# Performance work log

Hardware: AMD Instinct MI355X
Metric: run time of the kernel (lower is better)

## Reference

```python
import jax, jax.numpy as jnp
import numpy as np

N_NODES = 100000   # embedding table rows
FEAT = 512         # feat_dim F
BATCH = 8192       # seed nodes per batch
DEG = 32           # sampled neighbors per node (col 0 = self)
BN_EPS = 1e-5


def setup_inputs() -> dict:
    key = jax.random.key(0)
    ks = jax.random.split(key, 6)
    feat_table = jax.random.normal(ks[0], (N_NODES, FEAT), dtype=jnp.float32)
    W_gen = jax.random.normal(ks[1], (2 * FEAT, 2 * FEAT), dtype=jnp.float32) * 0.02
    weight1 = jax.random.normal(ks[2], (3 * FEAT, 3 * FEAT), dtype=jnp.float32) * 0.02
    gamma = jnp.ones((3 * FEAT,), dtype=jnp.float32)
    beta = jnp.zeros((3 * FEAT,), dtype=jnp.float32)
    nodes = jax.random.randint(ks[3], (BATCH,), 0, N_NODES, dtype=jnp.int32)
    neigh_idx = jax.random.randint(ks[4], (BATCH, DEG), 0, N_NODES, dtype=jnp.int32)
    neigh_idx = neigh_idx.at[:, 0].set(nodes)  # self node included, as in samp_neighs
    return {"feat_table": feat_table, "W_gen": W_gen, "weight1": weight1,
            "gamma": gamma, "beta": beta, "nodes": nodes, "neigh_idx": neigh_idx}


def _batchnorm_train(x, gamma, beta):
    # BatchNorm1d in training mode: biased batch statistics over axis 0
    mu = x.mean(axis=0)
    var = x.var(axis=0)
    return (x - mu) * jax.lax.rsqrt(var + BN_EPS) * gamma + beta


def _gen(x, W_gen):
    # generator module: raw = x @ W_gen, gen = relu(raw) (shape-preserving [B,2F])
    raw = x @ W_gen
    return jax.nn.relu(raw), raw


def reference(feat_table, W_gen, weight1, gamma, beta, nodes, neigh_idx):
    # self features: [B, F]
    self_feats = feat_table[nodes]
    # gather neighbor feats [B, K, F] and mean-pool (replaces dense mask.mm)
    neigh_feats = feat_table[neigh_idx]
    agg_feats = neigh_feats.mean(axis=1)                 # [B, F]
    cat_feats = jnp.concatenate([self_feats, agg_feats], axis=1)  # [B, 2F]
    gen_feats, raw_feats = _gen(cat_feats, W_gen)        # [B, 2F] each

    # environment aggregation: self node (column 0) removed from neighbor set
    env_agg_feats = neigh_feats[:, 1:, :].mean(axis=1)   # [B, F]
    env_cat = jnp.concatenate([jnp.zeros_like(self_feats), env_agg_feats], axis=1)
    env_gen_feats, env_raw_feats = _gen(env_cat, W_gen)

    # train_flag=True, rl_train_flag=False path
    feats = jnp.concatenate([agg_feats, gen_feats], axis=1)  # [B, 3F]
    to_feats = jax.nn.relu(_batchnorm_train(feats, gamma, beta) @ weight1)
    return (agg_feats, to_feats, gen_feats, raw_feats, env_gen_feats, env_raw_feats)
```

## Files before the change

### kernel.cpp

```cpp
#include <hip/hip_runtime.h>
#include <hip/hip_bf16.h>

typedef unsigned short u16;
typedef unsigned int u32;
typedef __attribute__((ext_vector_type(8))) short short8;
typedef __attribute__((ext_vector_type(4))) float f32x4;

#define BATCH 8192
#define FEAT 512
#define DEG 32
#define BM 128
#define BN 128
#define BK 32

__device__ __forceinline__ float b2f(u16 h){
  union { u32 u; float f; } x; x.u = ((u32)h) << 16; return x.f;
}
__device__ __forceinline__ u16 f2b(float f){
  __hip_bfloat16 h = __float2bfloat16(f);
  return *reinterpret_cast<u16*>(&h);
}
__device__ __forceinline__ u32 pack2(float lo, float hi){
  return (u32)f2b(lo) | (((u32)f2b(hi)) << 16);
}

__device__ __forceinline__ f32x4 mfma_bf16_16x16x32(short8 a, short8 b, f32x4 c){
  asm("v_mfma_f32_16x16x32_bf16 %0, %1, %2, %0" : "+v"(c) : "v"(a), "v"(b));
  return c;
}

__device__ __forceinline__ void gload16(const u16* g, u16* l){
  __builtin_amdgcn_global_load_lds(
      (const __attribute__((address_space(1))) u32*)(const void*)g,
      (__attribute__((address_space(3))) u32*)(void*)l, 16, 0, 0);
}

__global__ __launch_bounds__(256) void gather_agg(
    const float* __restrict__ feat, const int* __restrict__ nodes,
    const int* __restrict__ nidx, float* __restrict__ out_agg,
    u16* __restrict__ cat_bf, u16* __restrict__ env_bf)
{
  const int b = blockIdx.x;
  const int t = threadIdx.x;
  __shared__ int idx[DEG];
  __shared__ int self_node;
  if (t < DEG) idx[t] = nidx[b * DEG + t];
  if (t == 64) self_node = nodes[b];
  __syncthreads();
  const int f = t * 2;
  float s0 = 0.f, s1 = 0.f;
  #pragma unroll 8
  for (int k = 0; k < DEG; ++k){
    const float2 v = *(const float2*)(feat + (size_t)idx[k] * FEAT + f);
    s0 += v.x; s1 += v.y;
  }
  const float2 sv = *(const float2*)(feat + (size_t)self_node * FEAT + f);
  const float a0 = s0 * (1.f/32.f), a1 = s1 * (1.f/32.f);
  const float e0 = (s0 - sv.x) * (1.f/31.f), e1 = (s1 - sv.y) * (1.f/31.f);
  *(float2*)(out_agg + (size_t)b * FEAT + f) = make_float2(a0, a1);
  *(u32*)(cat_bf + (size_t)b * 1024 + f) = pack2(sv.x, sv.y);
  *(u32*)(cat_bf + (size_t)b * 1024 + FEAT + f) = pack2(a0, a1);
  *(u32*)(env_bf + (size_t)b * FEAT + f) = pack2(e0, e1);
}

__global__ __launch_bounds__(256) void transpose_f2b(
    const float* __restrict__ in, u16* __restrict__ out, int R, int C)
{
  __shared__ float tile[32][33];
  const int c0 = blockIdx.x * 32, r0 = blockIdx.y * 32;
  const int x = threadIdx.x, y = threadIdx.y;
  #pragma unroll
  for (int i = 0; i < 32; i += 8)
    tile[y + i][x] = in[(size_t)(r0 + y + i) * C + (c0 + x)];
  __syncthreads();
  #pragma unroll
  for (int i = 0; i < 32; i += 8)
    out[(size_t)(c0 + y + i) * R + (r0 + x)] = f2b(tile[x][y + i]);
}

template<bool WRITE_RAW>
__device__ __forceinline__ void gemm_body(
    const u16* __restrict__ A, int lda, const u16* __restrict__ BT, int ldb,
    int K, float* __restrict__ Craw, float* __restrict__ Crelu, int ldc,
    int m0, int n0, u16* As, u16* Bs)
{
  const int t = threadIdx.x;
  const int wave = t >> 6, lane = t & 63;
  const int wr = wave >> 1, wc = wave & 1;
  const int lm = lane & 15, quad = lane >> 4;

  const int sr = wave * 32 + (lane >> 2);
  const int sc = (lane & 3) * 8;

  f32x4 acc[4][4] = {};

  for (int k0 = 0; k0 < K; k0 += BK){
    gload16(A  + (size_t)(m0 + sr)      * lda + k0 + sc, As + sr * 32 + sc);
    gload16(A  + (size_t)(m0 + sr + 16) * lda + k0 + sc, As + (sr + 16) * 32 + sc);
    gload16(BT + (size_t)(n0 + sr)      * ldb + k0 + sc, Bs + sr * 32 + sc);
    gload16(BT + (size_t)(n0 + sr + 16) * ldb + k0 + sc, Bs + (sr + 16) * 32 + sc);
    __syncthreads();
    short8 af[4], bf[4];
    #pragma unroll
    for (int i = 0; i < 4; ++i)
      af[i] = *(const short8*)&As[(wr * 64 + i * 16 + lm) * 32 + quad * 8];
    #pragma unroll
    for (int j = 0; j < 4; ++j)
      bf[j] = *(const short8*)&Bs[(wc * 64 + j * 16 + lm) * 32 + quad * 8];
    #pragma unroll
    for (int i = 0; i < 4; ++i)
      #pragma unroll
      for (int j = 0; j < 4; ++j)
        acc[i][j] = mfma_bf16_16x16x32(af[i], bf[j], acc[i][j]);
    __syncthreads();
  }
  #pragma unroll
  for (int i = 0; i < 4; ++i){
    const int row = m0 + wr * 64 + i * 16 + quad * 4;
    #pragma unroll
    for (int j = 0; j < 4; ++j){
      const int col = n0 + wc * 64 + j * 16 + lm;
      #pragma unroll
      for (int r = 0; r < 4; ++r){
        const float v = acc[i][j][r];
        const size_t off = (size_t)(row + r) * ldc + col;
        if (WRITE_RAW) Craw[off] = v;
        Crelu[off] = fmaxf(v, 0.f);
      }
    }
  }
}

__global__ __launch_bounds__(256) void gemm12(
    const u16* __restrict__ catA, const u16* __restrict__ envA,
    const u16* __restrict__ wgT,
    float* __restrict__ raw, float* __restrict__ gen,
    float* __restrict__ envraw, float* __restrict__ envgen)
{
  __shared__ __align__(16) u16 As[BM * BK];
  __shared__ __align__(16) u16 Bs[BN * BK];
  const int z = blockIdx.z;
  const u16* A  = z ? envA : catA;
  const int lda = z ? 512 : 1024;
  const int K   = z ? 512 : 1024;
  const u16* BT = z ? wgT + 512 : wgT;
  float* Craw   = z ? envraw : raw;
  float* Crelu  = z ? envgen : gen;
  gemm_body<true>(A, lda, BT, 1024, K, Craw, Crelu, 1024,
                  blockIdx.y * BM, blockIdx.x * BN, As, Bs);
}

__global__ __launch_bounds__(256) void gemm3(
    const u16* __restrict__ bnA, const u16* __restrict__ w1T,
    float* __restrict__ to_out)
{
  __shared__ __align__(16) u16 As[BM * BK];
  __shared__ __align__(16) u16 Bs[BN * BK];
  gemm_body<false>(bnA, 1536, w1T, 1536, 1536, nullptr, to_out, 1536,
                   blockIdx.y * BM, blockIdx.x * BN, As, Bs);
}

__global__ __launch_bounds__(256) void zero_f32(float* __restrict__ p, int n){
  const int i = blockIdx.x * 256 + threadIdx.x;
  if (i < n) p[i] = 0.f;
}

__global__ __launch_bounds__(256) void bn_partial(
    const float* __restrict__ agg, const float* __restrict__ gen,
    float* __restrict__ sums)
{
  const int l = threadIdx.x & 63;
  const int ty = threadIdx.x >> 6;
  const int c = blockIdx.x * 64 + l;
  const int r0 = blockIdx.y * 1024;
  float s = 0.f, q = 0.f;
  if (c < 512){
    for (int r = r0 + ty; r < r0 + 1024; r += 4){
      const float x = agg[(size_t)r * 512 + c];
      s += x; q += x * x;
    }
  } else {
    for (int r = r0 + ty; r < r0 + 1024; r += 4){
      const float x = gen[(size_t)r * 1024 + (c - 512)];
      s += x; q += x * x;
    }
  }
  __shared__ float sh[2][4][64];
  sh[0][ty][l] = s; sh[1][ty][l] = q;
  __syncthreads();
  if (ty == 0){
    s = sh[0][0][l] + sh[0][1][l] + sh[0][2][l] + sh[0][3][l];
    q = sh[1][0][l] + sh[1][1][l] + sh[1][2][l] + sh[1][3][l];
    atomicAdd(&sums[c], s);
    atomicAdd(&sums[1536 + c], q);
  }
}

__global__ __launch_bounds__(256) void bn_finalize(
    const float* __restrict__ sums, const float* __restrict__ gamma,
    const float* __restrict__ beta, float* __restrict__ sArr, float* __restrict__ tArr)
{
  const int c = blockIdx.x * 256 + threadIdx.x;
  if (c >= 1536) return;
  const float mean = sums[c] * (1.f / 8192.f);
  const float var = sums[1536 + c] * (1.f / 8192.f) - mean * mean;
  const float rs = rsqrtf(var + 1e-5f);
  const float sc = gamma[c] * rs;
  sArr[c] = sc;
  tArr[c] = beta[c] - mean * sc;
}

__global__ __launch_bounds__(384) void prep_bnA(
    const float* __restrict__ agg, const float* __restrict__ gen,
    const float* __restrict__ sArr, const float* __restrict__ tArr,
    u16* __restrict__ bnA)
{
  const int m = blockIdx.x;
  const int t = threadIdx.x;
  const int c = t * 4;
  const float4 x = (c < 512)
      ? *(const float4*)(agg + (size_t)m * 512 + c)
      : *(const float4*)(gen + (size_t)m * 1024 + (c - 512));
  const float4 s4 = *(const float4*)(sArr + c);
  const float4 t4 = *(const float4*)(tArr + c);
  const u32 lo = pack2(fmaf(x.x, s4.x, t4.x), fmaf(x.y, s4.y, t4.y));
  const u32 hi = pack2(fmaf(x.z, s4.z, t4.z), fmaf(x.w, s4.w, t4.w));
  *(uint2*)(bnA + (size_t)m * 1536 + c) = make_uint2(lo, hi);
}

extern "C" void kernel_launch(void* const* d_in, const int* in_sizes, int n_in,
                              void* d_out, int out_size, void* d_ws, size_t ws_size,
                              hipStream_t stream)
{
  const float* feat  = (const float*)d_in[0];
  const float* Wgen  = (const float*)d_in[1];
  const float* W1    = (const float*)d_in[2];
  const float* gamma = (const float*)d_in[3];
  const float* beta  = (const float*)d_in[4];
  const int* nodes   = (const int*)d_in[5];
  const int* nidx    = (const int*)d_in[6];

  float* o = (float*)d_out;
  float* out_agg    = o;
  float* out_to     = o + 4194304;
  float* out_gen    = o + 16777216;
  float* out_raw    = o + 25165824;
  float* out_envgen = o + 33554432;
  float* out_envraw = o + 41943040;

  char* w = (char*)d_ws;
  float* sums = (float*)w;
  float* sArr = (float*)(w + 12288);
  float* tArr = (float*)(w + 18432);
  u16* wgT    = (u16*)(w + 32768);
  u16* w1T    = (u16*)(w + 2129920);
  u16* cat_bf = (u16*)(w + 6848512);
  u16* env_bf = (u16*)(w + 23625728);
  u16* bnA_bf = (u16*)(w + 6848512);

  gather_agg<<<BATCH, 256, 0, stream>>>(feat, nodes, nidx, out_agg, cat_bf, env_bf);
  transpose_f2b<<<dim3(32, 32), dim3(32, 8), 0, stream>>>(Wgen, wgT, 1024, 1024);
  transpose_f2b<<<dim3(48, 48), dim3(32, 8), 0, stream>>>(W1, w1T, 1536, 1536);

  gemm12<<<dim3(8, 64, 2), 256, 0, stream>>>(
      cat_bf, env_bf, wgT, out_raw, out_gen, out_envraw, out_envgen);

  zero_f32<<<12, 256, 0, stream>>>(sums, 3072);
  bn_partial<<<dim3(24, 8), 256, 0, stream>>>(out_agg, out_gen, sums);
  bn_finalize<<<6, 256, 0, stream>>>(sums, gamma, beta, sArr, tArr);
  prep_bnA<<<BATCH, 384, 0, stream>>>(out_agg, out_gen, sArr, tArr, bnA_bf);

  gemm3<<<dim3(12, 64), 256, 0, stream>>>(bnA_bf, w1T, out_to);
}
```

Baseline: 598.4 us.

## Rewrite GEMMs as 256x256 triple-buffered tiles; vectorize gather and BN stats

The GEMMs move to 256x256 tiles with 8 waves, triple-buffered LDS loads, an XOR-swizzled LDS layout and split MFMA phases with priority hints. Block IDs are remapped across XCDs. The gather kernel now handles two rows per block with float4 loads and takes the self row from neighbor column 0. The BN partial sums write per-slice partials instead of using atomics, which drops the zeroing kernel. The aim is better MFMA utilization and fewer memory and launch costs, at the price of more LDS and register pressure and fewer blocks.

```diff
diff --git a/kernel.cpp b/kernel.cpp
--- a/kernel.cpp
+++ b/kernel.cpp
@@ -9,13 +9,7 @@
 #define BATCH 8192
 #define FEAT 512
 #define DEG 32
-#define BM 128
-#define BN 128
-#define BK 32
-
-__device__ __forceinline__ float b2f(u16 h){
-  union { u32 u; float f; } x; x.u = ((u32)h) << 16; return x.f;
-}
+
 __device__ __forceinline__ u16 f2b(float f){
   __hip_bfloat16 h = __float2bfloat16(f);
   return *reinterpret_cast<u16*>(&h);
@@ -36,31 +30,31 @@
 }
 
 __global__ __launch_bounds__(256) void gather_agg(
-    const float* __restrict__ feat, const int* __restrict__ nodes,
-    const int* __restrict__ nidx, float* __restrict__ out_agg,
-    u16* __restrict__ cat_bf, u16* __restrict__ env_bf)
-{
-  const int b = blockIdx.x;
+    const float* __restrict__ feat, const int* __restrict__ nidx,
+    float* __restrict__ out_agg, u16* __restrict__ cat_bf, u16* __restrict__ env_bf)
+{
   const int t = threadIdx.x;
-  __shared__ int idx[DEG];
-  __shared__ int self_node;
-  if (t < DEG) idx[t] = nidx[b * DEG + t];
-  if (t == 64) self_node = nodes[b];
+  const int half = t >> 7, tl = t & 127;
+  const int b = blockIdx.x * 2 + half;
+  __shared__ int idx[2][DEG];
+  if (t < 2 * DEG)
+    idx[t >> 5][t & 31] = nidx[(size_t)(blockIdx.x * 2 + (t >> 5)) * DEG + (t & 31)];
   __syncthreads();
-  const int f = t * 2;
-  float s0 = 0.f, s1 = 0.f;
+  const int f = tl * 4;
+  const float4 sv = *(const float4*)(feat + (size_t)idx[half][0] * FEAT + f);
+  float4 s = sv;
   #pragma unroll 8
-  for (int k = 0; k < DEG; ++k){
-    const float2 v = *(const float2*)(feat + (size_t)idx[k] * FEAT + f);
-    s0 += v.x; s1 += v.y;
-  }
-  const float2 sv = *(const float2*)(feat + (size_t)self_node * FEAT + f);
-  const float a0 = s0 * (1.f/32.f), a1 = s1 * (1.f/32.f);
-  const float e0 = (s0 - sv.x) * (1.f/31.f), e1 = (s1 - sv.y) * (1.f/31.f);
-  *(float2*)(out_agg + (size_t)b * FEAT + f) = make_float2(a0, a1);
-  *(u32*)(cat_bf + (size_t)b * 1024 + f) = pack2(sv.x, sv.y);
-  *(u32*)(cat_bf + (size_t)b * 1024 + FEAT + f) = pack2(a0, a1);
-  *(u32*)(env_bf + (size_t)b * FEAT + f) = pack2(e0, e1);
+  for (int k = 1; k < DEG; ++k){
+    const float4 v = *(const float4*)(feat + (size_t)idx[half][k] * FEAT + f);
+    s.x += v.x; s.y += v.y; s.z += v.z; s.w += v.w;
+  }
+  const float4 a = make_float4(s.x*(1.f/32.f), s.y*(1.f/32.f), s.z*(1.f/32.f), s.w*(1.f/32.f));
+  const float4 e = make_float4((s.x-sv.x)*(1.f/31.f), (s.y-sv.y)*(1.f/31.f),
+                               (s.z-sv.z)*(1.f/31.f), (s.w-sv.w)*(1.f/31.f));
+  *(float4*)(out_agg + (size_t)b * FEAT + f) = a;
+  *(uint2*)(cat_bf + (size_t)b * 1024 + f)        = make_uint2(pack2(sv.x, sv.y), pack2(sv.z, sv.w));
+  *(uint2*)(cat_bf + (size_t)b * 1024 + FEAT + f) = make_uint2(pack2(a.x, a.y), pack2(a.z, a.w));
+  *(uint2*)(env_bf + (size_t)b * FEAT + f)        = make_uint2(pack2(e.x, e.y), pack2(e.z, e.w));
 }
 
 __global__ __launch_bounds__(256) void transpose_f2b(
@@ -79,44 +73,97 @@
 }
 
 template<bool WRITE_RAW>
-__device__ __forceinline__ void gemm_body(
+__device__ __forceinline__ void gemm_body8(
     const u16* __restrict__ A, int lda, const u16* __restrict__ BT, int ldb,
     int K, float* __restrict__ Craw, float* __restrict__ Crelu, int ldc,
-    int m0, int n0, u16* As, u16* Bs)
-{
-  const int t = threadIdx.x;
-  const int wave = t >> 6, lane = t & 63;
-  const int wr = wave >> 1, wc = wave & 1;
+    int m0, int n0, u16* __restrict__ As, u16* __restrict__ Bs)
+{
+  const int tid = threadIdx.x;
+  const int wave = tid >> 6, lane = tid & 63;
+  const int wr = wave >> 2, wc = wave & 3;
   const int lm = lane & 15, quad = lane >> 4;
 
-  const int sr = wave * 32 + (lane >> 2);
-  const int sc = (lane & 3) * 8;
-
-  f32x4 acc[4][4] = {};
-
-  for (int k0 = 0; k0 < K; k0 += BK){
-    gload16(A  + (size_t)(m0 + sr)      * lda + k0 + sc, As + sr * 32 + sc);
-    gload16(A  + (size_t)(m0 + sr + 16) * lda + k0 + sc, As + (sr + 16) * 32 + sc);
-    gload16(BT + (size_t)(n0 + sr)      * ldb + k0 + sc, Bs + sr * 32 + sc);
-    gload16(BT + (size_t)(n0 + sr + 16) * ldb + k0 + sc, Bs + (sr + 16) * 32 + sc);
-    __syncthreads();
-    short8 af[4], bf[4];
+  const int r0 = tid >> 2;
+  const int csrc = ((tid & 3) ^ ((r0 >> 1) & 3)) * 8;
+  const u16* aS = A  + (size_t)(m0 + r0) * lda + csrc;
+  const u16* bS = BT + (size_t)(n0 + r0) * ldb + csrc;
+  const size_t aU1 = (size_t)128 * lda, bU1 = (size_t)128 * ldb;
+  u16* dA = As + tid * 8;
+  u16* dB = Bs + tid * 8;
+
+  const int cs8 = (quad ^ ((lm >> 1) & 3)) * 8;
+  const u16* rA = As + (wr * 128 + lm) * 32 + cs8;
+  const u16* rB = Bs + (wc * 64  + lm) * 32 + cs8;
+
+  f32x4 acc[8][4] = {};
+
+  const int nt = K >> 5;
+  gload16(aS,            dA);
+  gload16(aS + aU1,      dA + 4096);
+  gload16(bS,            dB);
+  gload16(bS + bU1,      dB + 4096);
+  gload16(aS + 32,       dA + 8192);
+  gload16(aS + 32 + aU1, dA + 8192 + 4096);
+  gload16(bS + 32,       dB + 8192);
+  gload16(bS + 32 + bU1, dB + 8192 + 4096);
+  asm volatile("s_waitcnt vmcnt(4)" ::: "memory");
+  __builtin_amdgcn_s_barrier();
+
+  int cur = 0, nxt = 2;
+  int koff = 64;
+  for (int t = 0; t < nt; ++t){
+    const bool st = (t + 2) < nt;
+    const u16* rAc = rA + cur * 8192;
+    const u16* rBc = rB + cur * 8192;
+    short8 af[8], b0, b1;
     #pragma unroll
-    for (int i = 0; i < 4; ++i)
-      af[i] = *(const short8*)&As[(wr * 64 + i * 16 + lm) * 32 + quad * 8];
+    for (int i = 0; i < 8; ++i) af[i] = *(const short8*)(rAc + i * 512);
+    b0 = *(const short8*)(rBc);
+    b1 = *(const short8*)(rBc + 512);
+    if (st){
+      gload16(aS + koff, dA + nxt * 8192);
+      gload16(bS + koff, dB + nxt * 8192);
+    }
+    __builtin_amdgcn_s_barrier();
+    asm volatile("s_waitcnt lgkmcnt(0)" ::: "memory");
+    __builtin_amdgcn_sched_barrier(0);
+    __builtin_amdgcn_s_setprio(1);
     #pragma unroll
-    for (int j = 0; j < 4; ++j)
-      bf[j] = *(const short8*)&Bs[(wc * 64 + j * 16 + lm) * 32 + quad * 8];
+    for (int i = 0; i < 8; ++i){
+      acc[i][0] = mfma_bf16_16x16x32(af[i], b0, acc[i][0]);
+      acc[i][1] = mfma_bf16_16x16x32(af[i], b1, acc[i][1]);
+    }
+    __builtin_amdgcn_s_setprio(0);
+    __builtin_amdgcn_sched_barrier(0);
+    __builtin_amdgcn_s_barrier();
+    short8 b2 = *(const short8*)(rBc + 1024);
+    short8 b3 = *(const short8*)(rBc + 1536);
+    if (st){
+      gload16(aS + koff + aU1, dA + nxt * 8192 + 4096);
+      gload16(bS + koff + bU1, dB + nxt * 8192 + 4096);
+    }
+    __builtin_amdgcn_s_barrier();
+    asm volatile("s_waitcnt lgkmcnt(0)" ::: "memory");
+    __builtin_amdgcn_sched_barrier(0);
+    __builtin_amdgcn_s_setprio(1);
     #pragma unroll
-    for (int i = 0; i < 4; ++i)
-      #pragma unroll
-      for (int j = 0; j < 4; ++j)
-        acc[i][j] = mfma_bf16_16x16x32(af[i], bf[j], acc[i][j]);
-    __syncthreads();
-  }
+    for (int i = 0; i < 8; ++i){
+      acc[i][2] = mfma_bf16_16x16x32(af[i], b2, acc[i][2]);
+      acc[i][3] = mfma_bf16_16x16x32(af[i], b3, acc[i][3]);
+    }
+    __builtin_amdgcn_s_setprio(0);
+    if (st) asm volatile("s_waitcnt vmcnt(4)" ::: "memory");
+    else    asm volatile("s_waitcnt vmcnt(0)" ::: "memory");
+    __builtin_amdgcn_sched_barrier(0);
+    __builtin_amdgcn_s_barrier();
+    koff += 32;
+    cur = (cur == 2) ? 0 : cur + 1;
+    nxt = (nxt == 2) ? 0 : nxt + 1;
+  }
+
   #pragma unroll
-  for (int i = 0; i < 4; ++i){
-    const int row = m0 + wr * 64 + i * 16 + quad * 4;
+  for (int i = 0; i < 8; ++i){
+    const int row = m0 + wr * 128 + i * 16 + quad * 4;
     #pragma unroll
     for (int j = 0; j < 4; ++j){
       const int col = n0 + wc * 64 + j * 16 + lm;
@@ -131,79 +178,92 @@
   }
 }
 
-__global__ __launch_bounds__(256) void gemm12(
+__global__ __launch_bounds__(512, 2) void gemm12(
     const u16* __restrict__ catA, const u16* __restrict__ envA,
     const u16* __restrict__ wgT,
     float* __restrict__ raw, float* __restrict__ gen,
     float* __restrict__ envraw, float* __restrict__ envgen)
 {
-  __shared__ __align__(16) u16 As[BM * BK];
-  __shared__ __align__(16) u16 Bs[BN * BK];
-  const int z = blockIdx.z;
+  __shared__ __align__(16) u16 As[3 * 8192];
+  __shared__ __align__(16) u16 Bs[3 * 8192];
+  const int bid = blockIdx.x;
+  const int wg = (bid & 7) * 32 + (bid >> 3);
+  const int z = wg >> 7;
+  const int r = wg & 127;
+  const int m0 = (r >> 2) * 256;
+  const int n0 = (r & 3) * 256;
   const u16* A  = z ? envA : catA;
   const int lda = z ? 512 : 1024;
   const int K   = z ? 512 : 1024;
-  const u16* BT = z ? wgT + 512 : wgT;
+  const u16* B  = z ? wgT + 512 : wgT;
   float* Craw   = z ? envraw : raw;
   float* Crelu  = z ? envgen : gen;
-  gemm_body<true>(A, lda, BT, 1024, K, Craw, Crelu, 1024,
-                  blockIdx.y * BM, blockIdx.x * BN, As, Bs);
-}
-
-__global__ __launch_bounds__(256) void gemm3(
+  gemm_body8<true>(A, lda, B, 1024, K, Craw, Crelu, 1024, m0, n0, As, Bs);
+}
+
+__global__ __launch_bounds__(512, 2) void gemm3(
     const u16* __restrict__ bnA, const u16* __restrict__ w1T,
     float* __restrict__ to_out)
 {
-  __shared__ __align__(16) u16 As[BM * BK];
-  __shared__ __align__(16) u16 Bs[BN * BK];
-  gemm_body<false>(bnA, 1536, w1T, 1536, 1536, nullptr, to_out, 1536,
-                   blockIdx.y * BM, blockIdx.x * BN, As, Bs);
-}
-
-__global__ __launch_bounds__(256) void zero_f32(float* __restrict__ p, int n){
-  const int i = blockIdx.x * 256 + threadIdx.x;
-  if (i < n) p[i] = 0.f;
+  __shared__ __align__(16) u16 As[3 * 8192];
+  __shared__ __align__(16) u16 Bs[3 * 8192];
+  const int bid = blockIdx.x;
+  const int wg = (bid & 7) * 24 + (bid >> 3);
+  const int m0 = (wg / 6) * 256;
+  const int n0 = (wg % 6) * 256;
+  gemm_body8<false>(bnA, 1536, w1T, 1536, 1536, nullptr, to_out, 1536, m0, n0, As, Bs);
 }
 
 __global__ __launch_bounds__(256) void bn_partial(
     const float* __restrict__ agg, const float* __restrict__ gen,
-    float* __restrict__ sums)
-{
-  const int l = threadIdx.x & 63;
-  const int ty = threadIdx.x >> 6;
-  const int c = blockIdx.x * 64 + l;
+    float* __restrict__ partials)
+{
+  const int tq = threadIdx.x & 63, ty = threadIdx.x >> 6;
+  const int c = blockIdx.x * 256 + tq * 4;
   const int r0 = blockIdx.y * 1024;
-  float s = 0.f, q = 0.f;
+  float4 s = make_float4(0.f,0.f,0.f,0.f), q = make_float4(0.f,0.f,0.f,0.f);
   if (c < 512){
     for (int r = r0 + ty; r < r0 + 1024; r += 4){
-      const float x = agg[(size_t)r * 512 + c];
-      s += x; q += x * x;
+      const float4 x = *(const float4*)(agg + (size_t)r * 512 + c);
+      s.x += x.x; s.y += x.y; s.z += x.z; s.w += x.w;
+      q.x += x.x*x.x; q.y += x.y*x.y; q.z += x.z*x.z; q.w += x.w*x.w;
     }
   } else {
     for (int r = r0 + ty; r < r0 + 1024; r += 4){
-      const float x = gen[(size_t)r * 1024 + (c - 512)];
-      s += x; q += x * x;
-    }
-  }
-  __shared__ float sh[2][4][64];
-  sh[0][ty][l] = s; sh[1][ty][l] = q;
+      const float4 x = *(const float4*)(gen + (size_t)r * 1024 + (c - 512));
+      s.x += x.x; s.y += x.y; s.z += x.z; s.w += x.w;
+      q.x += x.x*x.x; q.y += x.y*x.y; q.z += x.z*x.z; q.w += x.w*x.w;
+    }
+  }
+  __shared__ float4 sh[2][4][64];
+  sh[0][ty][tq] = s; sh[1][ty][tq] = q;
   __syncthreads();
   if (ty == 0){
-    s = sh[0][0][l] + sh[0][1][l] + sh[0][2][l] + sh[0][3][l];
-    q = sh[1][0][l] + sh[1][1][l] + sh[1][2][l] + sh[1][3][l];
-    atomicAdd(&sums[c], s);
-    atomicAdd(&sums[1536 + c], q);
+    float4 s0 = sh[0][0][tq], s1 = sh[0][1][tq], s2 = sh[0][2][tq], s3 = sh[0][3][tq];
+    float4 q0 = sh[1][0][tq], q1 = sh[1][1][tq], q2 = sh[1][2][tq], q3 = sh[1][3][tq];
+    const float4 S = make_float4(s0.x+s1.x+s2.x+s3.x, s0.y+s1.y+s2.y+s3.y,
+                                 s0.z+s1.z+s2.z+s3.z, s0.w+s1.w+s2.w+s3.w);
+    const float4 Q = make_float4(q0.x+q1.x+q2.x+q3.x, q0.y+q1.y+q2.y+q3.y,
+                                 q0.z+q1.z+q2.z+q3.z, q0.w+q1.w+q2.w+q3.w);
+    *(float4*)(partials + (size_t)blockIdx.y * 3072 + c)        = S;
+    *(float4*)(partials + (size_t)blockIdx.y * 3072 + 1536 + c) = Q;
   }
 }
 
 __global__ __launch_bounds__(256) void bn_finalize(
-    const float* __restrict__ sums, const float* __restrict__ gamma,
+    const float* __restrict__ partials, const float* __restrict__ gamma,
     const float* __restrict__ beta, float* __restrict__ sArr, float* __restrict__ tArr)
 {
   const int c = blockIdx.x * 256 + threadIdx.x;
   if (c >= 1536) return;
-  const float mean = sums[c] * (1.f / 8192.f);
-  const float var = sums[1536 + c] * (1.f / 8192.f) - mean * mean;
+  float s = 0.f, q = 0.f;
+  #pragma unroll
+  for (int k = 0; k < 8; ++k){
+    s += partials[k * 3072 + c];
+    q += partials[k * 3072 + 1536 + c];
+  }
+  const float mean = s * (1.f / 8192.f);
+  const float var = q * (1.f / 8192.f) - mean * mean;
   const float rs = rsqrtf(var + 1e-5f);
   const float sc = gamma[c] * rs;
   sArr[c] = sc;
@@ -237,7 +297,6 @@
   const float* W1    = (const float*)d_in[2];
   const float* gamma = (const float*)d_in[3];
   const float* beta  = (const float*)d_in[4];
-  const int* nodes   = (const int*)d_in[5];
   const int* nidx    = (const int*)d_in[6];
 
   float* o = (float*)d_out;
@@ -249,26 +308,25 @@
   float* out_envraw = o + 41943040;
 
   char* w = (char*)d_ws;
-  float* sums = (float*)w;
   float* sArr = (float*)(w + 12288);
   float* tArr = (float*)(w + 18432);
   u16* wgT    = (u16*)(w + 32768);
+  float* partials = (float*)(w + 32768);
   u16* w1T    = (u16*)(w + 2129920);
   u16* cat_bf = (u16*)(w + 6848512);
   u16* env_bf = (u16*)(w + 23625728);
   u16* bnA_bf = (u16*)(w + 6848512);
 
-  gather_agg<<<BATCH, 256, 0, stream>>>(feat, nodes, nidx, out_agg, cat_bf, env_bf);
+  gather_agg<<<BATCH / 2, 256, 0, stream>>>(feat, nidx, out_agg, cat_bf, env_bf);
   transpose_f2b<<<dim3(32, 32), dim3(32, 8), 0, stream>>>(Wgen, wgT, 1024, 1024);
   transpose_f2b<<<dim3(48, 48), dim3(32, 8), 0, stream>>>(W1, w1T, 1536, 1536);
 
-  gemm12<<<dim3(8, 64, 2), 256, 0, stream>>>(
+  gemm12<<<256, 512, 0, stream>>>(
       cat_bf, env_bf, wgT, out_raw, out_gen, out_envraw, out_envgen);
 
-  zero_f32<<<12, 256, 0, stream>>>(sums, 3072);
-  bn_partial<<<dim3(24, 8), 256, 0, stream>>>(out_agg, out_gen, sums);
-  bn_finalize<<<6, 256, 0, stream>>>(sums, gamma, beta, sArr, tArr);
+  bn_partial<<<dim3(6, 8), 256, 0, stream>>>(out_agg, out_gen, partials);
+  bn_finalize<<<6, 256, 0, stream>>>(partials, gamma, beta, sArr, tArr);
   prep_bnA<<<BATCH, 384, 0, stream>>>(out_agg, out_gen, sArr, tArr, bnA_bf);
 
-  gemm3<<<dim3(12, 64), 256, 0, stream>>>(bnA_bf, w1T, out_to);
-}
+  gemm3<<<192, 512, 0, stream>>>(bnA_bf, w1T, out_to);
+}
```

Measured after the change: 622.6 us. 4.0% more time.
